# Kernel optimization log

Measured on AMD Instinct MI355X. Metric: run time of the kernel, lower is better.

The kernel has to match this reference:

```python
import jax, jax.numpy as jnp
import numpy as np

BATCH = 4096
FEAT = 1024
HID = 1024


def setup_inputs() -> dict:
    key = jax.random.key(0)
    ks = jax.random.split(key, 11)
    s_x = 1.0 / np.sqrt(FEAT)
    s_h = 1.0 / np.sqrt(HID)
    return {
        "x": jax.random.normal(ks[0], (BATCH, FEAT), jnp.float32),
        "h_prev": jax.random.normal(ks[1], (BATCH, HID), jnp.float32),
        "c_prev": jax.random.normal(ks[2], (BATCH, HID), jnp.float32),
        # Dense(3*hidden) on x and h (keras Dense: y = x @ W + b)
        "W_ifo_x": jax.random.normal(ks[3], (FEAT, 3 * HID), jnp.float32) * s_x,
        "b_ifo_x": jnp.zeros((3 * HID,), jnp.float32),
        "W_ifo_h": jax.random.normal(ks[4], (HID, 3 * HID), jnp.float32) * s_h,
        "b_ifo_h": jnp.zeros((3 * HID,), jnp.float32),
        # Dense(hidden) on x and h for candidate 'a'
        "W_b_x": jax.random.normal(ks[5], (FEAT, HID), jnp.float32) * s_x,
        "b_b_x": jnp.zeros((HID,), jnp.float32),
        "W_b_h": jax.random.normal(ks[6], (HID, HID), jnp.float32) * s_h,
        "b_b_h": jnp.zeros((HID,), jnp.float32),
    }


def reference(x, h_prev, c_prev, W_ifo_x, b_ifo_x, W_ifo_h, b_ifo_h,
              W_b_x, b_b_x, W_b_h, b_b_h):
    # Fused gate projections: [B, 3H]
    ifo = jax.nn.sigmoid(x @ W_ifo_x + b_ifo_x + h_prev @ W_ifo_h + b_ifo_h)
    i, f, o = jnp.split(ifo, 3, axis=-1)
    a = jnp.tanh(x @ W_b_x + b_b_x + h_prev @ W_b_h + b_b_h)
    c = i * a + f * c_prev
    h = o * jnp.tanh(c)
    return (h, c)
```

## Files before the change

### kernel.cpp

```cpp
#include <hip/hip_runtime.h>
#include <hip/hip_bf16.h>
#include <stdint.h>
#include <stddef.h>


#define BATCH 4096
#define FEAT  1024
#define HID   1024
#define NCAT  4096
#define KCAT  2048

typedef __attribute__((ext_vector_type(8))) __bf16 bf16x8;
typedef __attribute__((ext_vector_type(4))) float  floatx4;

__device__ __forceinline__ unsigned short f2bf(float f) {
    __hip_bfloat16 b = __float2bfloat16(f);
    return *reinterpret_cast<unsigned short*>(&b);
}

#define BM 256
#define BN 256
#define BK 64
#define NIT 16
#define HALF 8192

#define A_OFF(PAR, KS) (((PAR) * 2 + (KS)) * HALF)
#define B_OFF(PAR, KS) (32768 + ((PAR) * 2 + (KS)) * HALF)

#define ISSUE_A(S, KT, KS) {                                                    \
    const float* s_ = ((KT) < 16) ? (xrow + (KT) * 64 + (KS) * 32)              \
                                  : (hrow + ((KT) - 16) * 64 + (KS) * 32);      \
    S[0] = *(const floatx4*)(s_);      S[1] = *(const floatx4*)(s_ + 4);        \
    S[2] = *(const floatx4*)(s_ + 8);  S[3] = *(const floatx4*)(s_ + 12); }

#define COMMIT_A(S, PAR, KS) {                                                  \
    union { unsigned short u[8]; uint4 v; } w0_, w1_;                           \
    _Pragma("unroll")                                                           \
    for (int e_ = 0; e_ < 4; ++e_) {                                            \
        w0_.u[e_] = f2bf(S[0][e_]); w0_.u[4 + e_] = f2bf(S[1][e_]);             \
        w1_.u[e_] = f2bf(S[2][e_]); w1_.u[4 + e_] = f2bf(S[3][e_]); }           \
    *(uint4*)&lds[A_OFF(PAR, KS) + am * 32 + as0 * 8] = w0_.v;                  \
    *(uint4*)&lds[A_OFF(PAR, KS) + am * 32 + as1 * 8] = w1_.v; }

#define ISSUE_B(S, KT, KS) {                                                    \
    int kg_ = (KT) * 64 + (KS) * 32 + bk4;                                      \
    const float* s_ = (kg_ < 1024) ? (bxcol + (size_t)kg_ * bstride)            \
                                   : (bhcol + (size_t)(kg_ - 1024) * bstride);  \
    S[0] = *(const floatx4*)(s_);                                               \
    S[1] = *(const floatx4*)(s_ + bstride);                                     \
    S[2] = *(const floatx4*)(s_ + 2 * (size_t)bstride);                         \
    S[3] = *(const floatx4*)(s_ + 3 * (size_t)bstride); }

#define COMMIT_B(S, PAR, KS) {                                                  \
    _Pragma("unroll")                                                           \
    for (int c_ = 0; c_ < 4; ++c_) {                                            \
        union { unsigned short u[4]; uint2 v; } w_;                             \
        w_.u[0] = f2bf(S[0][c_]); w_.u[1] = f2bf(S[1][c_]);                     \
        w_.u[2] = f2bf(S[2][c_]); w_.u[3] = f2bf(S[3][c_]);                     \
        *(uint2*)&lds[B_OFF(PAR, KS) + (bnp4 + c_) * 32 + bswz * 8 + bsub * 4]  \
            = w_.v; } }

#define LOAD_BB(PAR, KS)                                                        \
    _Pragma("unroll")                                                           \
    for (int g_ = 0; g_ < 4; ++g_)                                              \
        bb[g_] = *(const bf16x8*)&lds[B_OFF(PAR, KS) + (wn + g_ * 16 + lm) * 32 + cr];
#define LOAD_AA(PAR, KS, IQ)                                                    \
    _Pragma("unroll")                                                           \
    for (int ii = 0; ii < 4; ++ii)                                              \
        aa[ii] = *(const bf16x8*)&lds[A_OFF(PAR, KS) + (wm + (IQ) * 64 + ii * 16 + lm) * 32 + cr];
#define MFMA16(IQ)                                                              \
    __builtin_amdgcn_s_setprio(1);                                              \
    _Pragma("unroll")                                                           \
    for (int ii = 0; ii < 4; ++ii)                                              \
        _Pragma("unroll")                                                       \
        for (int g_ = 0; g_ < 4; ++g_)                                          \
            acc[(IQ) * 4 + ii][g_] = __builtin_amdgcn_mfma_f32_16x16x32_bf16(   \
                aa[ii], bb[g_], acc[(IQ) * 4 + ii][g_], 0, 0, 0);               \
    __builtin_amdgcn_s_setprio(0);
#define BAR __builtin_amdgcn_s_barrier();
#define DRAIN asm volatile("s_waitcnt lgkmcnt(0)" ::: "memory");

__global__ __launch_bounds__(512, 2)
void lstm_one(const float* __restrict__ x, const float* __restrict__ h,
              const float* __restrict__ c_prev,
              const float* __restrict__ Wix, const float* __restrict__ Wih,
              const float* __restrict__ Wbx, const float* __restrict__ Wbh,
              const float* __restrict__ bix, const float* __restrict__ bih,
              const float* __restrict__ bbx, const float* __restrict__ bbh,
              float* __restrict__ out_h, float* __restrict__ out_c) {
    __shared__ unsigned short lds[65536];
    const int t    = threadIdx.x;
    const int lane = t & 63;
    const int wid  = t >> 6;
    const int wm   = (wid >> 2) * 128;
    const int wn   = (wid & 3) * 64;
    const int m0   = blockIdx.y * BM;
    const int n0   = blockIdx.x * BN;
    const int lm   = lane & 15;
    const int lk   = lane >> 4;
    const int cr   = (lk ^ ((lm >> 2) & 3)) * 8;

    const int am   = t >> 1;
    const float* xrow = x + (size_t)(m0 + am) * FEAT + (t & 1) * 16;
    const float* hrow = h + (size_t)(m0 + am) * HID  + (t & 1) * 16;
    const int ac0  = (t & 1) * 2;
    const int aswz = (am >> 2) & 3;
    const int as0  = ac0 ^ aswz;
    const int as1  = (ac0 + 1) ^ aswz;

    const int bnp4 = (t & 63) * 4;
    const int bk4  = (t >> 6) * 4;
    const int bg   = (bnp4 >> 4) & 3;
    const int bj   = (((n0 + bnp4) >> 6) << 4) | (bnp4 & 15);
    const int bq   = (bg < 3) ? bg * 1024 + bj : bj;
    const int bstride = (bg < 3) ? 3 * HID : HID;
    const float* bxcol = ((bg < 3) ? Wix : Wbx) + bq;
    const float* bhcol = ((bg < 3) ? Wih : Wbh) + bq;
    const int bswz = (bk4 >> 3) ^ ((bnp4 >> 2) & 3);
    const int bsub = (bk4 >> 2) & 1;

    floatx4 acc[8][4];
#pragma unroll
    for (int i = 0; i < 8; ++i)
#pragma unroll
        for (int g = 0; g < 4; ++g) acc[i][g] = (floatx4){0.f, 0.f, 0.f, 0.f};

    floatx4 SO[4], SE[4];
    bf16x8 aa[4], bb[4];

    ISSUE_A(SO, 0, 0) ISSUE_B(SE, 0, 0)
    COMMIT_A(SO, 0, 0) COMMIT_B(SE, 0, 0)
    ISSUE_A(SO, 0, 1) ISSUE_B(SE, 0, 1)
    COMMIT_A(SO, 0, 1) COMMIT_B(SE, 0, 1)
    ISSUE_A(SO, 1, 0) ISSUE_B(SE, 1, 0)
    COMMIT_A(SO, 1, 0) COMMIT_B(SE, 1, 0)
    ISSUE_A(SO, 1, 1)
    ISSUE_B(SE, 1, 1)
    DRAIN
    BAR

    for (int it = 0; it < NIT; ++it) {
        const int k2 = 2 * it + 2, k3 = 2 * it + 3;
        const bool more = (it < NIT - 1);

        COMMIT_A(SO, 1, 1) DRAIN
        LOAD_BB(0, 0) LOAD_AA(0, 0, 0)
        if (more) ISSUE_A(SO, k2, 0)
        BAR MFMA16(0) BAR
        COMMIT_B(SE, 1, 1) DRAIN
        LOAD_AA(0, 0, 1)
        if (more) ISSUE_B(SE, k2, 0)
        BAR MFMA16(1) BAR
        if (more) { COMMIT_A(SO, 0, 0) DRAIN }
        LOAD_BB(0, 1) LOAD_AA(0, 1, 0)
        if (more) ISSUE_A(SO, k2, 1)
        BAR MFMA16(0) BAR
        if (more) { COMMIT_B(SE, 0, 0) DRAIN }
        LOAD_AA(0, 1, 1)
        if (more) ISSUE_B(SE, k2, 1)
        BAR MFMA16(1) BAR
        if (more) { COMMIT_A(SO, 0, 1) DRAIN }
        LOAD_BB(1, 0) LOAD_AA(1, 0, 0)
        if (more) ISSUE_A(SO, k3, 0)
        BAR MFMA16(0) BAR
        if (more) { COMMIT_B(SE, 0, 1) DRAIN }
        LOAD_AA(1, 0, 1)
        if (more) ISSUE_B(SE, k3, 0)
        BAR MFMA16(1) BAR
        if (more) { COMMIT_A(SO, 1, 0) DRAIN }
        LOAD_BB(1, 1) LOAD_AA(1, 1, 0)
        if (more) ISSUE_A(SO, k3, 1)
        BAR MFMA16(0) BAR
        if (more) { COMMIT_B(SE, 1, 0) DRAIN }
        LOAD_AA(1, 1, 1)
        if (more) ISSUE_B(SE, k3, 1)
        BAR MFMA16(1) BAR
    }

    const int j  = (((n0 + wn) >> 6) << 4) + lm;
    const float bi = bix[j]           + bih[j];
    const float bf = bix[HID + j]     + bih[HID + j];
    const float bo = bix[2 * HID + j] + bih[2 * HID + j];
    const float ba = bbx[j]           + bbh[j];
#pragma unroll
    for (int i = 0; i < 8; ++i) {
#pragma unroll
        for (int r = 0; r < 4; ++r) {
            int m = m0 + wm + i * 16 + (lk * 4) + r;
            float pi = acc[i][0][r] + bi;
            float pf = acc[i][1][r] + bf;
            float po = acc[i][2][r] + bo;
            float pa = acc[i][3][r] + ba;
            float ig = 1.f / (1.f + __expf(-pi));
            float fg = 1.f / (1.f + __expf(-pf));
            float og = 1.f / (1.f + __expf(-po));
            float av = 2.f / (1.f + __expf(-2.f * pa)) - 1.f;
            float cp = c_prev[(size_t)m * HID + j];
            float cv = ig * av + fg * cp;
            float hv = og * (2.f / (1.f + __expf(-2.f * cv)) - 1.f);
            out_h[(size_t)m * HID + j] = hv;
            out_c[(size_t)m * HID + j] = cv;
        }
    }
}

extern "C" void kernel_launch(void* const* d_in, const int* in_sizes, int n_in,
                              void* d_out, int out_size, void* d_ws, size_t ws_size,
                              hipStream_t stream) {
    const float* x   = (const float*)d_in[0];
    const float* h   = (const float*)d_in[1];
    const float* c   = (const float*)d_in[2];
    const float* Wix = (const float*)d_in[3];
    const float* bix = (const float*)d_in[4];
    const float* Wih = (const float*)d_in[5];
    const float* bih = (const float*)d_in[6];
    const float* Wbx = (const float*)d_in[7];
    const float* bbx = (const float*)d_in[8];
    const float* Wbh = (const float*)d_in[9];
    const float* bbh = (const float*)d_in[10];

    float* out_h = (float*)d_out;
    float* out_c = out_h + (size_t)BATCH * HID;

    lstm_one<<<dim3(NCAT / BN, BATCH / BM), 512, 0, stream>>>(
        x, h, c, Wix, Wih, Wbx, Wbh, bix, bih, bbx, bbh, out_h, out_c);
}
```

Before: 209.0 us.

## Restructure B staging to scalar loads with 128-bit LDS stores and relaxed waits

Each thread now loads one weight column across 16 k-rows as scalar floats instead of four float4 rows, so it can pack 8 bf16 values per 128-bit LDS store in place of four 64-bit stores. The LDS swizzle for A and B is changed from (row>>2) to (row>>1) to fit the new write pattern. The full lgkmcnt(0) drains are replaced by partial waits placed just before the barrier, so LDS commits can overlap the fragment reads. The trade-off is more global load instructions for B (16 scalar loads instead of 4 vector loads), and the hand-picked wait counts must match the compiler's actual instruction counts to stay correct.

```diff
diff --git a/kernel.cpp b/kernel.cpp
--- a/kernel.cpp
+++ b/kernel.cpp
@@ -43,22 +43,22 @@
     *(uint4*)&lds[A_OFF(PAR, KS) + am * 32 + as1 * 8] = w1_.v; }
 
 #define ISSUE_B(S, KT, KS) {                                                    \
-    int kg_ = (KT) * 64 + (KS) * 32 + bk4;                                      \
-    const float* s_ = (kg_ < 1024) ? (bxcol + (size_t)kg_ * bstride)            \
-                                   : (bhcol + (size_t)(kg_ - 1024) * bstride);  \
-    S[0] = *(const floatx4*)(s_);                                               \
-    S[1] = *(const floatx4*)(s_ + bstride);                                     \
-    S[2] = *(const floatx4*)(s_ + 2 * (size_t)bstride);                         \
-    S[3] = *(const floatx4*)(s_ + 3 * (size_t)bstride); }
+    const int kb_ = (KT) * 64 + (KS) * 32;                                      \
+    const float* base_ = (kb_ < 1024)                                           \
+        ? (bxcol + (size_t)kb_ * bstride)                                       \
+        : (bhcol + (size_t)(kb_ - 1024) * bstride);                             \
+    _Pragma("unroll")                                                           \
+    for (int i_ = 0; i_ < 8; ++i_) {                                            \
+        S[i_]     = base_[(size_t)(bko + i_) * bstride];                        \
+        S[i_ + 8] = base_[(size_t)(bko + 16 + i_) * bstride]; } }
 
 #define COMMIT_B(S, PAR, KS) {                                                  \
-    _Pragma("unroll")                                                           \
-    for (int c_ = 0; c_ < 4; ++c_) {                                            \
-        union { unsigned short u[4]; uint2 v; } w_;                             \
-        w_.u[0] = f2bf(S[0][c_]); w_.u[1] = f2bf(S[1][c_]);                     \
-        w_.u[2] = f2bf(S[2][c_]); w_.u[3] = f2bf(S[3][c_]);                     \
-        *(uint2*)&lds[B_OFF(PAR, KS) + (bnp4 + c_) * 32 + bswz * 8 + bsub * 4]  \
-            = w_.v; } }
+    union { unsigned short u[8]; uint4 v; } w0_, w1_;                           \
+    _Pragma("unroll")                                                           \
+    for (int e_ = 0; e_ < 8; ++e_) {                                            \
+        w0_.u[e_] = f2bf(S[e_]); w1_.u[e_] = f2bf(S[e_ + 8]); }                 \
+    *(uint4*)&lds[B_OFF(PAR, KS) + bn * 32 + bs1 * 8] = w0_.v;                  \
+    *(uint4*)&lds[B_OFF(PAR, KS) + bn * 32 + bs2 * 8] = w1_.v; }
 
 #define LOAD_BB(PAR, KS)                                                        \
     _Pragma("unroll")                                                           \
@@ -78,7 +78,7 @@
                 aa[ii], bb[g_], acc[(IQ) * 4 + ii][g_], 0, 0, 0);               \
     __builtin_amdgcn_s_setprio(0);
 #define BAR __builtin_amdgcn_s_barrier();
-#define DRAIN asm volatile("s_waitcnt lgkmcnt(0)" ::: "memory");
+#define WAITK(N) asm volatile("s_waitcnt lgkmcnt(" #N ")" ::: "memory");
 
 __global__ __launch_bounds__(512, 2)
 void lstm_one(const float* __restrict__ x, const float* __restrict__ h,
@@ -98,26 +98,27 @@
     const int n0   = blockIdx.x * BN;
     const int lm   = lane & 15;
     const int lk   = lane >> 4;
-    const int cr   = (lk ^ ((lm >> 2) & 3)) * 8;
+    const int cr   = (lk ^ ((lm >> 1) & 3)) * 8;
 
     const int am   = t >> 1;
     const float* xrow = x + (size_t)(m0 + am) * FEAT + (t & 1) * 16;
     const float* hrow = h + (size_t)(m0 + am) * HID  + (t & 1) * 16;
     const int ac0  = (t & 1) * 2;
-    const int aswz = (am >> 2) & 3;
+    const int aswz = (am >> 1) & 3;
     const int as0  = ac0 ^ aswz;
     const int as1  = (ac0 + 1) ^ aswz;
 
-    const int bnp4 = (t & 63) * 4;
-    const int bk4  = (t >> 6) * 4;
-    const int bg   = (bnp4 >> 4) & 3;
-    const int bj   = (((n0 + bnp4) >> 6) << 4) | (bnp4 & 15);
+    const int bn   = ((t & 1) << 7) | ((t >> 1) & 127);
+    const int bo1  = (t >> 8) & 1;
+    const int bko  = bo1 * 8;
+    const int bg   = (bn >> 4) & 3;
+    const int bj   = (((n0 + bn) >> 6) << 4) | (bn & 15);
     const int bq   = (bg < 3) ? bg * 1024 + bj : bj;
     const int bstride = (bg < 3) ? 3 * HID : HID;
     const float* bxcol = ((bg < 3) ? Wix : Wbx) + bq;
     const float* bhcol = ((bg < 3) ? Wih : Wbh) + bq;
-    const int bswz = (bk4 >> 3) ^ ((bnp4 >> 2) & 3);
-    const int bsub = (bk4 >> 2) & 1;
+    const int bs1  = bo1 ^ ((bn >> 1) & 3);
+    const int bs2  = bs1 ^ 2;
 
     floatx4 acc[8][4];
 #pragma unroll
@@ -125,56 +126,57 @@
 #pragma unroll
         for (int g = 0; g < 4; ++g) acc[i][g] = (floatx4){0.f, 0.f, 0.f, 0.f};
 
-    floatx4 SO[4], SE[4];
+    floatx4 SO[4];
+    float   SB[16];
     bf16x8 aa[4], bb[4];
 
-    ISSUE_A(SO, 0, 0) ISSUE_B(SE, 0, 0)
-    COMMIT_A(SO, 0, 0) COMMIT_B(SE, 0, 0)
-    ISSUE_A(SO, 0, 1) ISSUE_B(SE, 0, 1)
-    COMMIT_A(SO, 0, 1) COMMIT_B(SE, 0, 1)
-    ISSUE_A(SO, 1, 0) ISSUE_B(SE, 1, 0)
-    COMMIT_A(SO, 1, 0) COMMIT_B(SE, 1, 0)
+    ISSUE_A(SO, 0, 0) ISSUE_B(SB, 0, 0)
+    COMMIT_A(SO, 0, 0) COMMIT_B(SB, 0, 0)
+    ISSUE_A(SO, 0, 1) ISSUE_B(SB, 0, 1)
+    COMMIT_A(SO, 0, 1) COMMIT_B(SB, 0, 1)
+    ISSUE_A(SO, 1, 0) ISSUE_B(SB, 1, 0)
+    COMMIT_A(SO, 1, 0) COMMIT_B(SB, 1, 0)
     ISSUE_A(SO, 1, 1)
-    ISSUE_B(SE, 1, 1)
-    DRAIN
+    ISSUE_B(SB, 1, 1)
+    WAITK(0)
     BAR
 
     for (int it = 0; it < NIT; ++it) {
         const int k2 = 2 * it + 2, k3 = 2 * it + 3;
         const bool more = (it < NIT - 1);
 
-        COMMIT_A(SO, 1, 1) DRAIN
+        COMMIT_A(SO, 1, 1)
         LOAD_BB(0, 0) LOAD_AA(0, 0, 0)
         if (more) ISSUE_A(SO, k2, 0)
-        BAR MFMA16(0) BAR
-        COMMIT_B(SE, 1, 1) DRAIN
+        WAITK(8) BAR MFMA16(0) BAR
+        COMMIT_B(SB, 1, 1)
         LOAD_AA(0, 0, 1)
-        if (more) ISSUE_B(SE, k2, 0)
-        BAR MFMA16(1) BAR
-        if (more) { COMMIT_A(SO, 0, 0) DRAIN }
+        if (more) ISSUE_B(SB, k2, 0)
+        WAITK(4) BAR MFMA16(1) BAR
+        if (more) { COMMIT_A(SO, 0, 0) }
         LOAD_BB(0, 1) LOAD_AA(0, 1, 0)
         if (more) ISSUE_A(SO, k2, 1)
-        BAR MFMA16(0) BAR
-        if (more) { COMMIT_B(SE, 0, 0) DRAIN }
+        WAITK(8) BAR MFMA16(0) BAR
+        if (more) { COMMIT_B(SB, 0, 0) }
         LOAD_AA(0, 1, 1)
-        if (more) ISSUE_B(SE, k2, 1)
-        BAR MFMA16(1) BAR
-        if (more) { COMMIT_A(SO, 0, 1) DRAIN }
+        if (more) ISSUE_B(SB, k2, 1)
+        WAITK(4) BAR MFMA16(1) BAR
+        if (more) { COMMIT_A(SO, 0, 1) }
         LOAD_BB(1, 0) LOAD_AA(1, 0, 0)
         if (more) ISSUE_A(SO, k3, 0)
-        BAR MFMA16(0) BAR
-        if (more) { COMMIT_B(SE, 0, 1) DRAIN }
+        WAITK(8) BAR MFMA16(0) BAR
+        if (more) { COMMIT_B(SB, 0, 1) }
         LOAD_AA(1, 0, 1)
-        if (more) ISSUE_B(SE, k3, 0)
-        BAR MFMA16(1) BAR
-        if (more) { COMMIT_A(SO, 1, 0) DRAIN }
+        if (more) ISSUE_B(SB, k3, 0)
+        WAITK(4) BAR MFMA16(1) BAR
+        if (more) { COMMIT_A(SO, 1, 0) }
         LOAD_BB(1, 1) LOAD_AA(1, 1, 0)
         if (more) ISSUE_A(SO, k3, 1)
-        BAR MFMA16(0) BAR
-        if (more) { COMMIT_B(SE, 1, 0) DRAIN }
+        WAITK(8) BAR MFMA16(0) BAR
+        if (more) { COMMIT_B(SB, 1, 0) }
         LOAD_AA(1, 1, 1)
-        if (more) ISSUE_B(SE, k3, 1)
-        BAR MFMA16(1) BAR
+        if (more) ISSUE_B(SB, k3, 1)
+        WAITK(4) BAR MFMA16(1) BAR
     }
 
     const int j  = (((n0 + wn) >> 6) << 4) + lm;
```

New measurement: 751.6 us. 3.6x slower.
